# Kernel tuning notes

Hardware: AMD Instinct MI355X
Metric: run time of the kernel (lower is better)

The kernel has to match this reference:

```python
import jax, jax.numpy as jnp
import numpy as np
from jax.scipy.special import logsumexp

B, L, M, D = 8192, 1024, 128, 2  # batch, hilbert.size, bond dim, local_size
MACHINE_POW = 2


def setup_inputs() -> dict:
    key = jax.random.key(0)
    k1, k2 = jax.random.split(key)
    # configurations in the zero-magnetization sector: each row is a permutation
    # of L//2 zeros and L//2 ones (constrained HomogeneousHilbert)
    base = jnp.tile(jnp.arange(D, dtype=jnp.int32), L // D)  # (L,)
    inputs = jax.vmap(lambda k: jax.random.permutation(k, base))(jax.random.split(k1, B))
    # variational parameters epsilon: (local_size, M, size); centered at 1 so the
    # length-L multiplicative cache chain stays in fp32 range
    epsilon = 1.0 + 0.02 * jax.random.normal(k2, (D, M, L), dtype=jnp.float32)
    return {"inputs": inputs, "epsilon": epsilon}


def _conditionals(inputs, epsilon):
    # inputs: (B, L) int in [0, D); epsilon: (D, M, L)
    Bn, Ln = inputs.shape
    Dn, Mn, _ = epsilon.shape
    half = Ln // 2

    def scan_fun(carry, index):
        cache, n_spins = carry                       # (B, D, M), (B, D)
        prev = inputs[:, (index - 1) % Ln]           # (B,) previous-site state
        params_i = epsilon[:, :, index]              # (D, M)
        # irregular gather: cache[b, prev[b], :]
        gathered = jnp.take_along_axis(cache, prev[:, None, None], axis=1)[:, 0, :]  # (B, M)
        prods = params_i[None, :, :] * gathered[:, None, :]  # (B, D, M)
        log_psi = jnp.sum(prods, axis=-1)            # (B, D) sum over bond dim
        n_spins = jnp.where(index > 0,
                            n_spins + jax.nn.one_hot(prev, Dn, dtype=jnp.int32),
                            n_spins)
        # zero-magnetization renormalization: -inf once a local state is exhausted
        renorm = jnp.log(jnp.heaviside((half - n_spins).astype(log_psi.dtype), 0.0))
        return (prods, n_spins), log_psi + renorm

    cache0 = jnp.ones((Bn, Dn, Mn), epsilon.dtype)
    n0 = jnp.zeros((Bn, Dn), jnp.int32)
    _, log_psi = jax.lax.scan(scan_fun, (cache0, n0), jnp.arange(Ln))
    return jnp.transpose(log_psi, (1, 0, 2))  # (B, L, D)


def reference(inputs, epsilon):
    lp = _conditionals(inputs, epsilon)  # (B, L, D)
    # normalize conditionals over local states (machine_pow = 2)
    lp = lp - (1.0 / MACHINE_POW) * logsumexp(MACHINE_POW * lp, axis=-1, keepdims=True)
    # pick the log-conditional of the actual configuration at each site
    sel = jnp.take_along_axis(lp, inputs[:, :, None], axis=2)[:, :, 0]  # (B, L)
    # n_symm = 1 (default apply_symmetries): symmetrized logsumexp is identity
    return jnp.sum(sel, axis=1)  # (B,) log_psi
```

## Files before the change

### kernel.cpp

```cpp
#include <hip/hip_runtime.h>
#include <hip/hip_fp16.h>

typedef unsigned long long u64;
typedef unsigned int uint32;
typedef short short8 __attribute__((ext_vector_type(8)));
typedef float f32x4 __attribute__((ext_vector_type(4)));
typedef _Float16 h2 __attribute__((ext_vector_type(2)));

#define B_N 8192
#define L_N 1024
#define M_N 128
#define HALF_N 512

#define OFF_WE   0x0
#define OFF_WO   0x20000
#define OFF_CMB  0x60000
#define OFF_LR   0xE0000
#define OFF_BITS 0x120000
#define OFF_T    0x220000
#define OFF_RQ   0x240000

#define PACK_BLK 2048
#define PACK_IT  16
#define EPS_BLK  32
#define ZERO_BLK 32

__device__ __forceinline__ unsigned short f32_bf16(float f) {
    union { float f; unsigned u; } x; x.f = f;
    unsigned u = x.u + 0x7FFFu + ((x.u >> 16) & 1u);
    return (unsigned short)(u >> 16);
}

__device__ __forceinline__ float fdot2(h2 a, h2 b, float c) {
#if __has_builtin(__builtin_amdgcn_fdot2)
    return __builtin_amdgcn_fdot2(a, b, c, false);
#else
    return (float)a[0] * (float)b[0] + (float)a[1] * (float)b[1] + c;
#endif
}

__device__ __forceinline__ uint32 fas_u(float f) { union { float f; uint32 u; } x; x.f = f; return x.u; }
__device__ __forceinline__ float uas_f(uint32 u) { union { uint32 u; float f; } x; x.u = u; return x.f; }

__device__ __forceinline__ float exp2_n(float x) {
#if __has_builtin(__builtin_amdgcn_exp2f)
    return __builtin_amdgcn_exp2f(x);
#else
    return exp2f(x);
#endif
}
__device__ __forceinline__ float log2_n(float x) {
#if __has_builtin(__builtin_amdgcn_logf)
    return __builtin_amdgcn_logf(x);
#else
    return __log2f(x);
#endif
}
__device__ __forceinline__ uint32 bfe1(uint32 v, int off) {
#if __has_builtin(__builtin_amdgcn_sbfe)
    return (uint32)__builtin_amdgcn_sbfe((int)v, off, 1);
#else
    return (uint32)((int)(v << (31 - off)) >> 31);
#endif
}
__device__ __forceinline__ uint32 ubfe2(uint32 v, int off) {
#if __has_builtin(__builtin_amdgcn_ubfe)
    return (uint32)__builtin_amdgcn_ubfe((int)v, off, 2);
#else
    return (v >> off) & 3u;
#endif
}

template<int CTRL>
__device__ __forceinline__ float dpp_add(float x, float y) {
    union { float f; int i; } a, r;
    a.f = y;
    r.i = __builtin_amdgcn_update_dpp(0, a.i, CTRL, 0xF, 0xF, true);
    return x + r.f;
}

union HU { uint32 u; __half2 hh; h2 v2; };

__global__ __launch_bounds__(256) void k_prep(const int* __restrict__ inp,
        const float* __restrict__ eps, u64* __restrict__ bits,
        _Float16* __restrict__ wE, _Float16* __restrict__ wO,
        _Float16* __restrict__ cmb,
        unsigned short* __restrict__ lrT, float* __restrict__ out) {
    int bid = blockIdx.x;
    if (bid < PACK_BLK) {
        int g = bid * 256 + threadIdx.x;
        const int stride = PACK_BLK * 256;
        #pragma unroll 4
        for (int it = 0; it < PACK_IT; ++it) {
            int v = inp[g];
            u64 m = __ballot(v != 0);
            if ((threadIdx.x & 63) == 0) bits[g >> 6] = m;
            g += stride;
        }
        return;
    }
    bid -= PACK_BLK;
    if (bid < EPS_BLK) {
        int wid = threadIdx.x >> 6, lane = threadIdx.x & 63;
        int m = bid * 4 + wid;
        const float* e0 = eps + (size_t)m * L_N + lane * 16;
        const float* e1 = eps + (size_t)(M_N + m) * L_N + lane * 16;
        float a[16], b[16];
        #pragma unroll
        for (int j = 0; j < 16; j += 4) {
            *(float4*)&a[j] = *(const float4*)&e0[j];
            *(float4*)&b[j] = *(const float4*)&e1[j];
        }
        float local = 1.f;
        #pragma unroll
        for (int j = 0; j < 16; ++j) local *= a[j];
        float sc = local;
        #pragma unroll
        for (int d = 1; d < 64; d <<= 1) {
            float up = __shfl_up(sc, d);
            if (lane >= d) sc *= up;
        }
        float prev = __shfl_up(sc, 1);
        float E = (lane == 0) ? 1.f : prev;
        int i0 = lane * 16;
        float rat_e = 1.f;
        #pragma unroll
        for (int j = 0; j < 16; ++j) {
            float rat = b[j] / a[j];
            float w = E * (a[j] - b[j]);
            lrT[(size_t)m * L_N + i0 + j] = f32_bf16(__log2f(rat));
            int u = (i0 + j) >> 1;
            if ((j & 1) == 0) {
                wE[(size_t)u * M_N + m] = (_Float16)w;
                rat_e = rat;
            } else {
                _Float16* wo = wO + (size_t)u * 2 * M_N;
                wo[m]       = (_Float16)w;
                wo[M_N + m] = (_Float16)(w * rat_e);
                _Float16* cr = cmb + (size_t)u * 4 * M_N;
                cr[m]           = (_Float16)0.f;
                cr[M_N + m]     = (_Float16)(rat_e - 1.f);
                cr[2*M_N + m]   = (_Float16)(rat - 1.f);
                cr[3*M_N + m]   = (_Float16)(rat_e * rat - 1.f);
            }
            E *= a[j];
        }
        return;
    }
    bid -= EPS_BLK;
    if (bid < ZERO_BLK) {
        out[bid * 256 + threadIdx.x] = 0.f;
    }
}

template<int CN>
__global__ __launch_bounds__(256) void k_slog2(const u64* __restrict__ bits,
        const unsigned short* __restrict__ lrT, _Float16* __restrict__ Rq,
        int* __restrict__ T) {
    if (blockIdx.x >= 1024) {
        int b = (blockIdx.x - 1024) * 256 + threadIdx.x;
        const u64* brow = bits + (size_t)b * 16;
        int n1 = 0, n0 = 0, Tv = 1024;
        for (int wd = 0; wd < 16; ++wd) {
            u64 x = brow[wd];
            int pc = __popcll(x);
            if (n1 + pc < HALF_N && n0 + (64 - pc) < HALF_N) {
                n1 += pc; n0 += 64 - pc;
                continue;
            }
            int found = 0;
            for (int k = 0; k < 64; ++k) {
                if (n1 >= HALF_N || n0 >= HALF_N) { Tv = wd * 64 + k; found = 1; break; }
                int sb = (int)((x >> k) & 1);
                n1 += sb; n0 += 1 - sb;
            }
            if (!found) Tv = (wd + 1) * 64;
            break;
        }
        T[b] = Tv;
        return;
    }
    int btile = blockIdx.x >> 1;
    int half = blockIdx.x & 1;
    int wid = threadIdx.x >> 6, lane = threadIdx.x & 63;
    int col = lane & 15, quad = lane >> 4;
    int m = (half * 4 + wid) * 16 + col;
    int b_row = btile * 16 + col;
    const u64* brow = bits + (size_t)b_row * 16;
    const unsigned short* lrow = lrT + (size_t)m * L_N;

    f32x4 cum = (f32x4){0.f, 0.f, 0.f, 0.f};

    for (int w = 0; w < 16; ++w) {
        u64 wv = brow[w];
        #pragma unroll
        for (int hf = 0; hf < 2; ++hf) {
            if (CN == 32 || hf == 0) {
                int cc = (CN == 32) ? (w * 2 + hf) : w;
                #pragma unroll
                for (int reg = 0; reg < 4; ++reg) {
                    int b = btile * 16 + quad * 4 + reg;
                    Rq[((size_t)cc * B_N + b) * M_N + m] = (_Float16)exp2_n(cum[reg]);
                }
            }
            short8 a;
            #pragma unroll
            for (int j = 0; j < 8; ++j)
                a[j] = (short)((((wv >> (hf * 32 + quad * 8 + j)) & 1) != 0) ? 0x3F80 : 0);
            union { uint4 u; short8 s; } bf;
            bf.u = *(const uint4*)(lrow + w * 64 + hf * 32 + quad * 8);
            cum = __builtin_amdgcn_mfma_f32_16x16x32_bf16(a, bf.s, cum, 0, 0, 0);
        }
    }
}

template<int CN>
__global__ __launch_bounds__(256) __attribute__((amdgpu_waves_per_eu(1, 4)))
void k_main(const u64* __restrict__ bits, const _Float16* __restrict__ wE,
        const _Float16* __restrict__ wO, const _Float16* __restrict__ cmb,
        const _Float16* __restrict__ Rq, const int* __restrict__ T,
        float* __restrict__ out) {
    constexpr int CHN = L_N / CN;
    constexpr int PRS = CHN / 2;
    constexpr int CSH = (CN == 16) ? 4 : 5;
    constexpr int NE  = PRS * M_N / (8 * 256);
    __shared__ _Float16 webuf[PRS * M_N];
    __shared__ _Float16 wobuf[PRS * 2 * M_N];
    __shared__ _Float16 cbuf [PRS * 4 * M_N];
    int c = blockIdx.x & (CN - 1);
    int bblk = blockIdx.x >> CSH;
    int lane = threadIdx.x & 63, wid = threadIdx.x >> 6;
    int s = lane & 7, grp = lane >> 3;
    int q = s & 3;
    int b0 = bblk * 128 + wid * 32 + grp * 4;

    {
        const uint4* se = (const uint4*)(wE  + (size_t)c * PRS * M_N);
        const uint4* so = (const uint4*)(wO  + (size_t)c * PRS * 2 * M_N);
        const uint4* sc = (const uint4*)(cmb + (size_t)c * PRS * 4 * M_N);
        uint4* de = (uint4*)webuf; uint4* dd = (uint4*)wobuf; uint4* dc = (uint4*)cbuf;
        #pragma unroll
        for (int t = 0; t < NE; ++t)     de[threadIdx.x + t * 256] = se[threadIdx.x + t * 256];
        #pragma unroll
        for (int t = 0; t < 2 * NE; ++t) dd[threadIdx.x + t * 256] = so[threadIdx.x + t * 256];
        #pragma unroll
        for (int t = 0; t < 4 * NE; ++t) dc[threadIdx.x + t * 256] = sc[threadIdx.x + t * 256];
    }

    HU R2[4][8];
    u64 wb[4];
    const int word0 = (c * CHN) >> 6;
    const int hs0 = (c * CHN >> 5) & 1;
    #pragma unroll
    for (int k = 0; k < 4; ++k) {
        int b = b0 + (q ^ k);
        union { uint4 v[2]; uint32 w[8]; } P;
        const uint4* src = (const uint4*)(Rq + ((size_t)c * B_N + b) * M_N + s * 16);
        P.v[0] = src[0]; P.v[1] = src[1];
        #pragma unroll
        for (int j = 0; j < 8; ++j) R2[k][j].u = P.w[j];
        wb[k] = bits[(size_t)b * 16 + word0];
    }
    int Tb = T[b0 + q];

    __syncthreads();

    const float LOG2E2 = 2.885390082f;
    const float NHL2 = -0.3465735903f;
    float sum = 0.f;
    #pragma unroll
    for (int h = 0; h < CHN / 32; ++h) {
        int sh = ((hs0 + h) & 1) * 32;
        uint32 wh[4];
        #pragma unroll
        for (int k = 0; k < 4; ++k) wh[k] = (uint32)(wb[k] >> sh);
        uint32 ows = ~wh[0];
        int rel = Tb - (c * CHN + h * 32);
        uint32 vmask = (rel <= 0) ? 0u : ((rel >= 32) ? 0xFFFFFFFFu : ((1u << rel) - 1u));

        #pragma unroll 2
        for (int tt = 0; tt < 16; ++tt) {
            int p = h * 16 + tt;
            union U8 { uint4 q4[2]; uint32 w[8]; h2 v2[8]; __half2 hh[8]; };
            U8 WEu;
            const _Float16* web = &webuf[p * M_N + s * 16];
            WEu.q4[0] = *(const uint4*)web;
            WEu.q4[1] = *((const uint4*)web + 1);

            uint32 cbo[4];
            #pragma unroll
            for (int k = 0; k < 4; ++k) cbo[k] = ubfe2(wh[k], 2 * tt);

            float de[4];
            #pragma unroll
            for (int k = 0; k < 4; ++k) {
                float acc = 0.f;
                #pragma unroll
                for (int j = 0; j < 8; ++j) acc = fdot2(R2[k][j].v2, WEu.v2[j], acc);
                de[k] = acc;
            }
            float dd[4];
            #pragma unroll
            for (int k = 0; k < 4; ++k) {
                U8 WOu;
                int ob = p * 2 * M_N + (int)((cbo[k] & 1u) << 7) + s * 16;
                WOu.q4[0] = *(const uint4*)&wobuf[ob];
                WOu.q4[1] = *((const uint4*)&wobuf[ob] + 1);
                float acc = 0.f;
                #pragma unroll
                for (int j = 0; j < 8; ++j) acc = fdot2(R2[k][j].v2, WOu.v2[j], acc);
                dd[k] = acc;
            }
            float xe = dpp_add<0xB1>(de[0], de[1]);
            float ye = dpp_add<0xB1>(de[2], de[3]);
            float De = dpp_add<0x4E>(xe, ye);
            De = dpp_add<0x104>(De, De);
            float xo = dpp_add<0xB1>(dd[0], dd[1]);
            float yo = dpp_add<0xB1>(dd[2], dd[3]);
            float Do = dpp_add<0x4E>(xo, yo);
            Do = dpp_add<0x104>(Do, Do);

            uint32 sg0 = bfe1(ows, 2 * tt) & 0x80000000u;
            float y0 = uas_f(fas_u(De) ^ sg0);
            float c0 = NHL2 * log2_n(1.f + exp2_n(LOG2E2 * y0));
            sum += uas_f(fas_u(c0) & bfe1(vmask, 2 * tt));
            uint32 sg1 = bfe1(ows, 2 * tt + 1) & 0x80000000u;
            float y1 = uas_f(fas_u(Do) ^ sg1);
            float c1 = NHL2 * log2_n(1.f + exp2_n(LOG2E2 * y1));
            sum += uas_f(fas_u(c1) & bfe1(vmask, 2 * tt + 1));

            #pragma unroll
            for (int k = 0; k < 4; ++k) {
                U8 CMu;
                int cb = p * 4 * M_N + (int)(cbo[k] << 7) + s * 16;
                CMu.q4[0] = *(const uint4*)&cbuf[cb];
                CMu.q4[1] = *((const uint4*)&cbuf[cb] + 1);
                #pragma unroll
                for (int j = 0; j < 8; ++j)
                    R2[k][j].hh = __hfma2(CMu.hh[j], R2[k][j].hh, R2[k][j].hh);
            }
        }
    }
    if (s < 4) atomicAdd(&out[b0 + s], sum);
}

extern "C" void kernel_launch(void* const* d_in, const int* in_sizes, int n_in,
                              void* d_out, int out_size, void* d_ws, size_t ws_size,
                              hipStream_t stream) {
    const int*   inputs  = (const int*)d_in[0];
    const float* epsilon = (const float*)d_in[1];
    float* out = (float*)d_out;

    char* ws = (char*)d_ws;
    _Float16* wE  = (_Float16*)(ws + OFF_WE);
    _Float16* wO  = (_Float16*)(ws + OFF_WO);
    _Float16* cmb = (_Float16*)(ws + OFF_CMB);
    unsigned short* lrT = (unsigned short*)(ws + OFF_LR);
    u64*   bits   = (u64*)  (ws + OFF_BITS);
    int*   T      = (int*)  (ws + OFF_T);
    _Float16* Rq  = (_Float16*)(ws + OFF_RQ);

    k_prep<<<PACK_BLK + EPS_BLK + ZERO_BLK, 256, 0, stream>>>(
        inputs, epsilon, bits, wE, wO, cmb, lrT, out);

    const size_t need32 = (size_t)OFF_RQ + (size_t)32 * B_N * M_N * 2;
    if (ws_size >= need32) {
        k_slog2<32><<<1024 + 32, 256, 0, stream>>>(bits, lrT, Rq, T);
        k_main<32><<<(B_N / 128) * 32, 256, 0, stream>>>(bits, wE, wO, cmb, Rq, T, out);
    } else {
        k_slog2<16><<<1024 + 32, 256, 0, stream>>>(bits, lrT, Rq, T);
        k_main<16><<<(B_N / 128) * 16, 256, 0, stream>>>(bits, wE, wO, cmb, Rq, T, out);
    }
}
```

Baseline: 163.4 us.

## Interleave odd-site weights with combine factors and stage LDS per half-chunk

Precomputed odd-site weights and cache-update factors are merged into one interleaved table, indexed directly by the 2-bit pair code. This replaces the separate wO and cmb tables and saves address arithmetic. The main kernel now stages only 16 site pairs into shared memory per 32-site half, reloading each half behind block barriers, which shrinks the LDS footprint and may raise occupancy. In exchange it adds an extra barrier and reload per half, and duplicates weight storage. The softplus accumulation is also folded into an fma.

```diff
diff --git a/kernel.cpp b/kernel.cpp
--- a/kernel.cpp
+++ b/kernel.cpp
@@ -13,12 +13,11 @@
 #define HALF_N 512
 
 #define OFF_WE   0x0
-#define OFF_WO   0x20000
-#define OFF_CMB  0x60000
-#define OFF_LR   0xE0000
-#define OFF_BITS 0x120000
-#define OFF_T    0x220000
-#define OFF_RQ   0x240000
+#define OFF_CW   0x20000
+#define OFF_LR   0x120000
+#define OFF_BITS 0x160000
+#define OFF_T    0x260000
+#define OFF_RQ   0x280000
 
 #define PACK_BLK 2048
 #define PACK_IT  16
@@ -83,8 +82,7 @@
 
 __global__ __launch_bounds__(256) void k_prep(const int* __restrict__ inp,
         const float* __restrict__ eps, u64* __restrict__ bits,
-        _Float16* __restrict__ wE, _Float16* __restrict__ wO,
-        _Float16* __restrict__ cmb,
+        _Float16* __restrict__ wE, _Float16* __restrict__ cw,
         unsigned short* __restrict__ lrT, float* __restrict__ out) {
     int bid = blockIdx.x;
     if (bid < PACK_BLK) {
@@ -123,7 +121,7 @@
         float prev = __shfl_up(sc, 1);
         float E = (lane == 0) ? 1.f : prev;
         int i0 = lane * 16;
-        float rat_e = 1.f;
+        float rat_e = 1.f, w_e = 0.f;
         #pragma unroll
         for (int j = 0; j < 16; ++j) {
             float rat = b[j] / a[j];
@@ -134,17 +132,20 @@
                 wE[(size_t)u * M_N + m] = (_Float16)w;
                 rat_e = rat;
             } else {
-                _Float16* wo = wO + (size_t)u * 2 * M_N;
-                wo[m]       = (_Float16)w;
-                wo[M_N + m] = (_Float16)(w * rat_e);
-                _Float16* cr = cmb + (size_t)u * 4 * M_N;
-                cr[m]           = (_Float16)0.f;
-                cr[M_N + m]     = (_Float16)(rat_e - 1.f);
-                cr[2*M_N + m]   = (_Float16)(rat - 1.f);
-                cr[3*M_N + m]   = (_Float16)(rat_e * rat - 1.f);
+                _Float16* cr = cw + (size_t)u * 4 * 256;
+                float wo1 = w * rat_e;
+                cr[0 * 256 + m]       = (_Float16)0.f;
+                cr[0 * 256 + 128 + m] = (_Float16)w;
+                cr[1 * 256 + m]       = (_Float16)(rat_e - 1.f);
+                cr[1 * 256 + 128 + m] = (_Float16)wo1;
+                cr[2 * 256 + m]       = (_Float16)(rat - 1.f);
+                cr[2 * 256 + 128 + m] = (_Float16)w;
+                cr[3 * 256 + m]       = (_Float16)(rat_e * rat - 1.f);
+                cr[3 * 256 + 128 + m] = (_Float16)wo1;
             }
             E *= a[j];
         }
+        (void)w_e;
         return;
     }
     bid -= EPS_BLK;
@@ -217,16 +218,12 @@
 template<int CN>
 __global__ __launch_bounds__(256) __attribute__((amdgpu_waves_per_eu(1, 4)))
 void k_main(const u64* __restrict__ bits, const _Float16* __restrict__ wE,
-        const _Float16* __restrict__ wO, const _Float16* __restrict__ cmb,
-        const _Float16* __restrict__ Rq, const int* __restrict__ T,
-        float* __restrict__ out) {
+        const _Float16* __restrict__ cw, const _Float16* __restrict__ Rq,
+        const int* __restrict__ T, float* __restrict__ out) {
     constexpr int CHN = L_N / CN;
-    constexpr int PRS = CHN / 2;
     constexpr int CSH = (CN == 16) ? 4 : 5;
-    constexpr int NE  = PRS * M_N / (8 * 256);
-    __shared__ _Float16 webuf[PRS * M_N];
-    __shared__ _Float16 wobuf[PRS * 2 * M_N];
-    __shared__ _Float16 cbuf [PRS * 4 * M_N];
+    __shared__ _Float16 webuf[16 * M_N];
+    __shared__ _Float16 cwbuf[16 * 4 * 256];
     int c = blockIdx.x & (CN - 1);
     int bblk = blockIdx.x >> CSH;
     int lane = threadIdx.x & 63, wid = threadIdx.x >> 6;
@@ -234,23 +231,10 @@
     int q = s & 3;
     int b0 = bblk * 128 + wid * 32 + grp * 4;
 
-    {
-        const uint4* se = (const uint4*)(wE  + (size_t)c * PRS * M_N);
-        const uint4* so = (const uint4*)(wO  + (size_t)c * PRS * 2 * M_N);
-        const uint4* sc = (const uint4*)(cmb + (size_t)c * PRS * 4 * M_N);
-        uint4* de = (uint4*)webuf; uint4* dd = (uint4*)wobuf; uint4* dc = (uint4*)cbuf;
-        #pragma unroll
-        for (int t = 0; t < NE; ++t)     de[threadIdx.x + t * 256] = se[threadIdx.x + t * 256];
-        #pragma unroll
-        for (int t = 0; t < 2 * NE; ++t) dd[threadIdx.x + t * 256] = so[threadIdx.x + t * 256];
-        #pragma unroll
-        for (int t = 0; t < 4 * NE; ++t) dc[threadIdx.x + t * 256] = sc[threadIdx.x + t * 256];
-    }
-
     HU R2[4][8];
     u64 wb[4];
     const int word0 = (c * CHN) >> 6;
-    const int hs0 = (c * CHN >> 5) & 1;
+    const int hs0 = ((c * CHN) >> 5) & 1;
     #pragma unroll
     for (int k = 0; k < 4; ++k) {
         int b = b0 + (q ^ k);
@@ -263,13 +247,23 @@
     }
     int Tb = T[b0 + q];
 
-    __syncthreads();
-
     const float LOG2E2 = 2.885390082f;
     const float NHL2 = -0.3465735903f;
     float sum = 0.f;
     #pragma unroll
     for (int h = 0; h < CHN / 32; ++h) {
+        if (h) __syncthreads();
+        {
+            size_t pbase = (size_t)c * (CHN / 2) + h * 16;
+            const uint4* se = (const uint4*)(wE + pbase * M_N);
+            const uint4* sc = (const uint4*)(cw + pbase * 4 * 256);
+            ((uint4*)webuf)[threadIdx.x] = se[threadIdx.x];
+            #pragma unroll
+            for (int t = 0; t < 8; ++t)
+                ((uint4*)cwbuf)[threadIdx.x + t * 256] = sc[threadIdx.x + t * 256];
+        }
+        __syncthreads();
+
         int sh = ((hs0 + h) & 1) * 32;
         uint32 wh[4];
         #pragma unroll
@@ -280,16 +274,17 @@
 
         #pragma unroll 2
         for (int tt = 0; tt < 16; ++tt) {
-            int p = h * 16 + tt;
             union U8 { uint4 q4[2]; uint32 w[8]; h2 v2[8]; __half2 hh[8]; };
             U8 WEu;
-            const _Float16* web = &webuf[p * M_N + s * 16];
+            const _Float16* web = &webuf[tt * M_N + s * 16];
             WEu.q4[0] = *(const uint4*)web;
             WEu.q4[1] = *((const uint4*)web + 1);
 
-            uint32 cbo[4];
-            #pragma unroll
-            for (int k = 0; k < 4; ++k) cbo[k] = ubfe2(wh[k], 2 * tt);
+            int pb = tt * 1024 + s * 16;
+            int ad[4];
+            #pragma unroll
+            for (int k = 0; k < 4; ++k)
+                ad[k] = pb + (int)(ubfe2(wh[k], 2 * tt) << 8);
 
             float de[4];
             #pragma unroll
@@ -303,9 +298,8 @@
             #pragma unroll
             for (int k = 0; k < 4; ++k) {
                 U8 WOu;
-                int ob = p * 2 * M_N + (int)((cbo[k] & 1u) << 7) + s * 16;
-                WOu.q4[0] = *(const uint4*)&wobuf[ob];
-                WOu.q4[1] = *((const uint4*)&wobuf[ob] + 1);
+                WOu.q4[0] = *(const uint4*)&cwbuf[ad[k] + 128];
+                WOu.q4[1] = *((const uint4*)&cwbuf[ad[k] + 128] + 1);
                 float acc = 0.f;
                 #pragma unroll
                 for (int j = 0; j < 8; ++j) acc = fdot2(R2[k][j].v2, WOu.v2[j], acc);
@@ -321,20 +315,17 @@
             Do = dpp_add<0x104>(Do, Do);
 
             uint32 sg0 = bfe1(ows, 2 * tt) & 0x80000000u;
-            float y0 = uas_f(fas_u(De) ^ sg0);
-            float c0 = NHL2 * log2_n(1.f + exp2_n(LOG2E2 * y0));
-            sum += uas_f(fas_u(c0) & bfe1(vmask, 2 * tt));
+            float l0 = log2_n(1.f + exp2_n(LOG2E2 * uas_f(fas_u(De) ^ sg0)));
+            sum = fmaf(NHL2, uas_f(fas_u(l0) & bfe1(vmask, 2 * tt)), sum);
             uint32 sg1 = bfe1(ows, 2 * tt + 1) & 0x80000000u;
-            float y1 = uas_f(fas_u(Do) ^ sg1);
-            float c1 = NHL2 * log2_n(1.f + exp2_n(LOG2E2 * y1));
-            sum += uas_f(fas_u(c1) & bfe1(vmask, 2 * tt + 1));
+            float l1 = log2_n(1.f + exp2_n(LOG2E2 * uas_f(fas_u(Do) ^ sg1)));
+            sum = fmaf(NHL2, uas_f(fas_u(l1) & bfe1(vmask, 2 * tt + 1)), sum);
 
             #pragma unroll
             for (int k = 0; k < 4; ++k) {
                 U8 CMu;
-                int cb = p * 4 * M_N + (int)(cbo[k] << 7) + s * 16;
-                CMu.q4[0] = *(const uint4*)&cbuf[cb];
-                CMu.q4[1] = *((const uint4*)&cbuf[cb] + 1);
+                CMu.q4[0] = *(const uint4*)&cwbuf[ad[k]];
+                CMu.q4[1] = *((const uint4*)&cwbuf[ad[k]] + 1);
                 #pragma unroll
                 for (int j = 0; j < 8; ++j)
                     R2[k][j].hh = __hfma2(CMu.hh[j], R2[k][j].hh, R2[k][j].hh);
@@ -353,22 +344,21 @@
 
     char* ws = (char*)d_ws;
     _Float16* wE  = (_Float16*)(ws + OFF_WE);
-    _Float16* wO  = (_Float16*)(ws + OFF_WO);
-    _Float16* cmb = (_Float16*)(ws + OFF_CMB);
+    _Float16* cw  = (_Float16*)(ws + OFF_CW);
     unsigned short* lrT = (unsigned short*)(ws + OFF_LR);
     u64*   bits   = (u64*)  (ws + OFF_BITS);
     int*   T      = (int*)  (ws + OFF_T);
     _Float16* Rq  = (_Float16*)(ws + OFF_RQ);
 
     k_prep<<<PACK_BLK + EPS_BLK + ZERO_BLK, 256, 0, stream>>>(
-        inputs, epsilon, bits, wE, wO, cmb, lrT, out);
+        inputs, epsilon, bits, wE, cw, lrT, out);
 
     const size_t need32 = (size_t)OFF_RQ + (size_t)32 * B_N * M_N * 2;
     if (ws_size >= need32) {
         k_slog2<32><<<1024 + 32, 256, 0, stream>>>(bits, lrT, Rq, T);
-        k_main<32><<<(B_N / 128) * 32, 256, 0, stream>>>(bits, wE, wO, cmb, Rq, T, out);
+        k_main<32><<<(B_N / 128) * 32, 256, 0, stream>>>(bits, wE, cw, Rq, T, out);
     } else {
         k_slog2<16><<<1024 + 32, 256, 0, stream>>>(bits, lrT, Rq, T);
-        k_main<16><<<(B_N / 128) * 16, 256, 0, stream>>>(bits, wE, wO, cmb, Rq, T, out);
-    }
-}
+        k_main<16><<<(B_N / 128) * 16, 256, 0, stream>>>(bits, wE, cw, Rq, T, out);
+    }
+}
```

Measured after the change: 162.5 us. No clear change (-0.6%).
